# Optimization experiments

Measured on AMD Instinct MI355X. Metric: run time of the kernel, lower is better.

The kernel has to match this reference:

```python
import jax, jax.numpy as jnp
import numpy as np

E, T_MAX, H, L, V = 384, 256, 6, 6, 65
DH = E // H  # 64
EPS = 1e-5


def setup_inputs() -> dict:
    key = jax.random.key(0)
    ks = jax.random.split(key, 24)
    B, T = 128, 256
    s = 0.02
    inp = {
        "input_indices": jax.random.randint(ks[0], (B, T), 0, V, dtype=jnp.int64) if jax.config.read("jax_enable_x64") else jax.random.randint(ks[0], (B, T), 0, V, dtype=jnp.int32),
        "targets": jax.random.randint(ks[1], (B, T), 0, V, dtype=jnp.int32),
        "tok_emb": s * jax.random.normal(ks[2], (V, E), jnp.float32),
        "pos_emb": s * jax.random.normal(ks[3], (T_MAX, E), jnp.float32),
        "Wq": s * jax.random.normal(ks[4], (L, H, E, DH), jnp.float32),
        "Wk": s * jax.random.normal(ks[5], (L, H, E, DH), jnp.float32),
        "Wv": s * jax.random.normal(ks[6], (L, H, E, DH), jnp.float32),
        "Wo": s * jax.random.normal(ks[7], (L, E, E), jnp.float32),
        "bo": jnp.zeros((L, E), jnp.float32),
        "ln1_s": jnp.ones((L, E), jnp.float32),
        "ln1_b": jnp.zeros((L, E), jnp.float32),
        "ln2_s": jnp.ones((L, E), jnp.float32),
        "ln2_b": jnp.zeros((L, E), jnp.float32),
        "W1": s * jax.random.normal(ks[8], (L, E, 4 * E), jnp.float32),
        "b1": jnp.zeros((L, 4 * E), jnp.float32),
        "W2": s * jax.random.normal(ks[9], (L, 4 * E, E), jnp.float32),
        "b2": jnp.zeros((L, E), jnp.float32),
        "lnf_s": jnp.ones((E,), jnp.float32),
        "lnf_b": jnp.zeros((E,), jnp.float32),
        "Wout": s * jax.random.normal(ks[10], (E, V), jnp.float32),
        "bout": jnp.zeros((V,), jnp.float32),
    }
    return inp


def _ln(x, s, b):
    m = x.mean(-1, keepdims=True)
    v = ((x - m) ** 2).mean(-1, keepdims=True)
    return (x - m) * jax.lax.rsqrt(v + EPS) * s + b


def _forward(input_indices, targets, tok_emb, pos_emb, Wq, Wk, Wv, Wo, bo,
             ln1_s, ln1_b, ln2_s, ln2_b, W1, b1, W2, b2, lnf_s, lnf_b, Wout, bout):
    B, T = input_indices.shape
    x = tok_emb[input_indices] + pos_emb[:T]  # [B,T,E]
    causal = jnp.tril(jnp.ones((T, T), bool))
    scale = DH ** -0.5

    def block(x, p):
        wq, wk, wv, wo, bo_, l1s, l1b, l2s, l2b, w1, b1_, w2, b2_ = p
        h = _ln(x, l1s, l1b)
        q = jnp.einsum("bte,hed->bhtd", h, wq)
        k = jnp.einsum("bte,hed->bhtd", h, wk)
        v = jnp.einsum("bte,hed->bhtd", h, wv)
        scores = jnp.einsum("bhtd,bhsd->bhts", q, k) * scale
        scores = jnp.where(causal, scores, -jnp.inf)
        w = jax.nn.softmax(scores, axis=-1)
        att = jnp.einsum("bhts,bhsd->bhtd", w, v)  # [B,H,T,DH]
        att = att.transpose(0, 2, 1, 3).reshape(B, T, E)  # concat heads
        x = x + att @ wo + bo_
        h2 = _ln(x, l2s, l2b)
        ff = jax.nn.relu(h2 @ w1 + b1_) @ w2 + b2_
        return x + ff, None

    x, _ = jax.lax.scan(block, x, (Wq, Wk, Wv, Wo, bo, ln1_s, ln1_b, ln2_s, ln2_b, W1, b1, W2, b2))
    x = _ln(x, lnf_s, lnf_b)
    logits = x @ Wout + bout  # [B,T,V]
    logp = jax.nn.log_softmax(logits, axis=-1)
    nll = -jnp.take_along_axis(logp, targets[..., None], axis=-1)[..., 0]
    loss = nll.mean()
    return logits, loss


def reference(input_indices, targets, tok_emb, pos_emb, Wq, Wk, Wv, Wo, bo,
              ln1_s, ln1_b, ln2_s, ln2_b, W1, b1, W2, b2, lnf_s, lnf_b, Wout, bout):
    return _forward(input_indices, targets, tok_emb, pos_emb, Wq, Wk, Wv, Wo, bo,
                    ln1_s, ln1_b, ln2_s, ln2_b, W1, b1, W2, b2, lnf_s, lnf_b, Wout, bout)
```

## Files before the change

### kernel.cpp

```cpp
#include <hip/hip_runtime.h>

#define BT      32768
#define T_SEQ   256
#define E_DIM   384
#define NH      6
#define NL      6
#define VOC     65
#define FF_DIM  1536
#define QKV_N   1152

typedef short bf16x8 __attribute__((ext_vector_type(8)));
typedef float f32x4  __attribute__((ext_vector_type(4)));
typedef unsigned short u16;

typedef const unsigned int __attribute__((address_space(1))) gu32;
typedef unsigned int       __attribute__((address_space(3))) lu32;

__device__ __forceinline__ u16 f2bf(float x) {
  unsigned u = __builtin_bit_cast(unsigned, x);
  u += 0x7fffu + ((u >> 16) & 1u);
  return (u16)(u >> 16);
}
__device__ __forceinline__ float bf2f(u16 v) {
  unsigned u = ((unsigned)v) << 16;
  return __builtin_bit_cast(float, u);
}

__device__ __forceinline__ void load_lds_16(const void* g, void* l) {
  __builtin_amdgcn_global_load_lds((gu32*)g, (lu32*)l, 16, 0, 0);
}

__global__ __launch_bounds__(256) void transpose_t(
    const float* __restrict__ src, u16* __restrict__ dst, int R, int C,
    long sbs, long dbs_outer, int inner, long dbs_inner, long dbase) {
  __shared__ float t[32][33];
  const int b = blockIdx.z;
  const float* s = src + (long)b * sbs;
  u16* d = dst + dbase + (long)(b / inner) * dbs_outer + (long)(b % inner) * dbs_inner;
  const int r0 = blockIdx.x * 32, c0 = blockIdx.y * 32;
  const int tx = threadIdx.x & 31, ty = threadIdx.x >> 5;
#pragma unroll
  for (int i = 0; i < 4; i++) {
    int rr = ty + i * 8;
    int r = r0 + rr, c = c0 + tx;
    if (r < R && c < C) t[rr][tx] = s[(long)r * C + c];
  }
  __syncthreads();
#pragma unroll
  for (int i = 0; i < 4; i++) {
    int cc = ty + i * 8;
    int c = c0 + cc, r = r0 + tx;
    if (c < C && r < R) d[(long)c * R + r] = f2bf(t[tx][cc]);
  }
}

__global__ __launch_bounds__(256) void embed_k(const int* __restrict__ idx,
                                               const float* __restrict__ tok,
                                               const float* __restrict__ pos,
                                               u16* __restrict__ x) {
  int i = blockIdx.x * 256 + threadIdx.x;
  int bt = i / 48, q = i - bt * 48;
  int t = bt & 255;
  const float4* tp = (const float4*)(tok + (size_t)idx[bt] * E_DIM + q * 8);
  const float4* pp = (const float4*)(pos + (size_t)t * E_DIM + q * 8);
  float4 a0 = tp[0], a1 = tp[1], p0 = pp[0], p1 = pp[1];
  u16 o[8];
  o[0] = f2bf(a0.x + p0.x); o[1] = f2bf(a0.y + p0.y);
  o[2] = f2bf(a0.z + p0.z); o[3] = f2bf(a0.w + p0.w);
  o[4] = f2bf(a1.x + p1.x); o[5] = f2bf(a1.y + p1.y);
  o[6] = f2bf(a1.z + p1.z); o[7] = f2bf(a1.w + p1.w);
  *(bf16x8*)(x + (size_t)bt * E_DIM + q * 8) = *(bf16x8*)o;
}

__global__ __launch_bounds__(256) void ln_k(const u16* __restrict__ x,
                                            const float* __restrict__ gam,
                                            const float* __restrict__ bet,
                                            u16* __restrict__ out) {
  int tid = threadIdx.x, lane = tid & 63, w = tid >> 6;
  size_t token = (size_t)blockIdx.x * 4 + w;
  const u16* xr = x + token * E_DIM;
  u16 raw[6];
  *(uint2*)raw          = *(const uint2*)(xr + 4 * lane);
  *(unsigned*)(raw + 4) = *(const unsigned*)(xr + 256 + 2 * lane);
  float v[6]; float s = 0.f;
#pragma unroll
  for (int i = 0; i < 6; i++) { v[i] = bf2f(raw[i]); s += v[i]; }
#pragma unroll
  for (int d = 1; d < 64; d <<= 1) s += __shfl_xor(s, d);
  float mean = s * (1.f / E_DIM);
  float q = 0.f;
#pragma unroll
  for (int i = 0; i < 6; i++) { float d0 = v[i] - mean; q += d0 * d0; }
#pragma unroll
  for (int d = 1; d < 64; d <<= 1) q += __shfl_xor(q, d);
  float r = rsqrtf(q * (1.f / E_DIM) + 1e-5f);
  int e[6] = {4 * lane, 4 * lane + 1, 4 * lane + 2, 4 * lane + 3,
              256 + 2 * lane, 256 + 2 * lane + 1};
  u16 o[6];
#pragma unroll
  for (int i = 0; i < 6; i++)
    o[i] = f2bf((v[i] - mean) * r * gam[e[i]] + bet[e[i]]);
  u16* orow = out + token * E_DIM;
  *(uint2*)(orow + 4 * lane)          = *(uint2*)o;
  *(unsigned*)(orow + 256 + 2 * lane) = *(unsigned*)(o + 4);
}

__global__ __launch_bounds__(256) void gemm_d(
    const u16* __restrict__ A, const u16* __restrict__ Bt, int K, int Nstore,
    const float* __restrict__ bias, const u16* __restrict__ resid,
    u16* __restrict__ outH, float* __restrict__ outF, int relu) {
  __shared__ u16 smem[16384];
  u16* As = smem;
  u16* Bs = smem + 8192;
  const int tid = threadIdx.x, lane = tid & 63, wv = tid >> 6;
  const int quad = lane >> 4, l16 = lane & 15;
  const int m0 = blockIdx.x * 128, n0 = blockIdx.y * 128;
  const int wm = (wv & 1) * 64, wn = (wv >> 1) * 64;

  const int lrow = lane >> 2;
  const int lchunk = (lane & 3) ^ ((lane >> 3) & 3);

  f32x4 acc[4][4];
#pragma unroll
  for (int i = 0; i < 4; i++)
#pragma unroll
    for (int j = 0; j < 4; j++) acc[i][j] = (f32x4){0.f, 0.f, 0.f, 0.f};

  auto stage = [&](int sel, int k0) {
#pragma unroll
    for (int j = 0; j < 2; j++) {
      int rid = wv * 2 + j;
      int r = rid * 16 + lrow;
      load_lds_16(A + (size_t)(m0 + r) * K + k0 + lchunk * 8, &As[sel * 4096 + rid * 512]);
      load_lds_16(Bt + (size_t)(n0 + r) * K + k0 + lchunk * 8, &Bs[sel * 4096 + rid * 512]);
    }
  };

  const int NK = K >> 5;
  stage(0, 0);
  __syncthreads();
  const int slot = (quad ^ ((l16 >> 1) & 3)) * 8;
  for (int kt = 0; kt < NK; kt++) {
    const int cur = kt & 1;
    if (kt + 1 < NK) stage(cur ^ 1, (kt + 1) * 32);
    const u16* Ab = As + cur * 4096;
    const u16* Bb = Bs + cur * 4096;
    bf16x8 af[4], bfr[4];
#pragma unroll
    for (int i = 0; i < 4; i++) af[i]  = *(const bf16x8*)&Ab[(wm + i * 16 + l16) * 32 + slot];
#pragma unroll
    for (int j = 0; j < 4; j++) bfr[j] = *(const bf16x8*)&Bb[(wn + j * 16 + l16) * 32 + slot];
#pragma unroll
    for (int i = 0; i < 4; i++)
#pragma unroll
      for (int j = 0; j < 4; j++)
        acc[i][j] = __builtin_amdgcn_mfma_f32_16x16x32_bf16(af[i], bfr[j], acc[i][j], 0, 0, 0);
    __syncthreads();
  }

  if (outH) {
#pragma unroll
    for (int p = 0; p < 4; p++) {
      if (p) __syncthreads();
      if ((wv >> 1) == (p >> 1)) {
#pragma unroll
        for (int jj = 0; jj < 2; jj++) {
          int j = (p & 1) * 2 + jj;
          int gn = n0 + wn + j * 16 + l16;
          float bv = bias ? bias[gn] : 0.f;
          int lcol = jj * 16 + l16;
#pragma unroll
          for (int i = 0; i < 4; i++)
#pragma unroll
            for (int r = 0; r < 4; r++) {
              float v = acc[i][j][r] + bv;
              if (relu) v = fmaxf(v, 0.f);
              smem[(wm + i * 16 + quad * 4 + r) * 36 + lcol] = f2bf(v);
            }
        }
      }
      __syncthreads();
      const int gc0 = n0 + p * 32;
#pragma unroll
      for (int s = 0; s < 4; s++) {
        int row = s * 32 + (tid >> 3);
        int seg = (tid & 7) * 4;
        u16 pk[4];
        *(uint2*)pk = *(const uint2*)&smem[row * 36 + seg];
        size_t o = (size_t)(m0 + row) * Nstore + gc0 + seg;
        if (resid) {
          u16 rv[4];
          *(uint2*)rv = *(const uint2*)&resid[o];
#pragma unroll
          for (int q2 = 0; q2 < 4; q2++) pk[q2] = f2bf(bf2f(pk[q2]) + bf2f(rv[q2]));
        }
        *(uint2*)&outH[o] = *(uint2*)pk;
      }
    }
  } else {
#pragma unroll
    for (int j = 0; j < 4; j++) {
      const int gn = n0 + wn + j * 16 + l16;
      if (gn < Nstore) {
        const float bv = bias ? bias[gn] : 0.f;
#pragma unroll
        for (int i = 0; i < 4; i++)
#pragma unroll
          for (int r = 0; r < 4; r++) {
            const int gm = m0 + wm + i * 16 + quad * 4 + r;
            outF[(size_t)gm * Nstore + gn] = acc[i][j][r] + bv;
          }
      }
    }
  }
}

__global__ __launch_bounds__(512) void attn_k(const u16* __restrict__ qkv,
                                              u16* __restrict__ att) {
  __shared__ u16 Kc[64 * 64];
  __shared__ u16 Vtc[64 * 64];
  __shared__ u16 Pl[8 * 16 * 64];
  const int b = blockIdx.x / NH, h = blockIdx.x % NH;
  const int tid = threadIdx.x, lane = tid & 63, w = tid >> 6;
  const int quad = lane >> 4, l16 = lane & 15;
  const int rowb = b * T_SEQ;
  const int tiles[2] = {w, 15 - w};

  bf16x8 qf[2][2];
#pragma unroll
  for (int ti = 0; ti < 2; ti++)
#pragma unroll
    for (int kk = 0; kk < 2; kk++)
      qf[ti][kk] = *(const bf16x8*)(qkv + (size_t)(rowb + tiles[ti] * 16 + l16) * QKV_N +
                                    h * 64 + kk * 32 + quad * 8);

  f32x4 Oa[2][4];
  float mrun[2][4], lrun[2][4];
#pragma unroll
  for (int ti = 0; ti < 2; ti++) {
#pragma unroll
    for (int di = 0; di < 4; di++) Oa[ti][di] = (f32x4){0.f, 0.f, 0.f, 0.f};
#pragma unroll
    for (int r = 0; r < 4; r++) { mrun[ti][r] = -1e30f; lrun[ti][r] = 0.f; }
  }

  u16* Pw = &Pl[w * 1024];
  const int sr = tid >> 3, sseg = tid & 7;
  const int kst = sseg ^ (sr & 7) ^ ((sr >> 3) & 7);

  for (int c = 0; c < 4; c++) {
    const int s0 = c * 64;
    __syncthreads();
    *(uint4*)&Kc[sr * 64 + kst * 8] =
        *(const uint4*)(qkv + (size_t)(rowb + s0 + sr) * QKV_N + 384 + h * 64 + sseg * 8);
    {
      union { uint4 u; u16 us[8]; } tb;
      tb.u = *(const uint4*)(qkv + (size_t)(rowb + s0 + sr) * QKV_N + 768 + h * 64 + sseg * 8);
#pragma unroll
      for (int j = 0; j < 8; j++) {
        int d = sseg * 8 + j;
        int vst = (sr >> 3) ^ (d & 7) ^ ((d >> 3) & 7);
        Vtc[d * 64 + vst * 8 + (sr & 7)] = tb.us[j];
      }
    }
    __syncthreads();

    bf16x8 kf[4][2], vf[4][2];
    bool loaded = false;
#pragma unroll
    for (int ti = 0; ti < 2; ti++) {
      const int t = tiles[ti];
      if (t < 4 * c) continue;
      if (!loaded) {
        loaded = true;
#pragma unroll
        for (int ni = 0; ni < 4; ni++)
#pragma unroll
          for (int kk = 0; kk < 2; kk++) {
            int srow = ni * 16 + l16;
            int ks = (kk * 4 + quad) ^ (srow & 7) ^ ((srow >> 3) & 7);
            kf[ni][kk] = *(const bf16x8*)&Kc[srow * 64 + ks * 8];
            int drow = ni * 16 + l16;
            int vs = (kk * 4 + quad) ^ (drow & 7) ^ ((drow >> 3) & 7);
            vf[ni][kk] = *(const bf16x8*)&Vtc[drow * 64 + vs * 8];
          }
      }
      f32x4 S[4];
#pragma unroll
      for (int ni = 0; ni < 4; ni++) {
        f32x4 z = (f32x4){0.f, 0.f, 0.f, 0.f};
        z = __builtin_amdgcn_mfma_f32_16x16x32_bf16(qf[ti][0], kf[ni][0], z, 0, 0, 0);
        S[ni] = __builtin_amdgcn_mfma_f32_16x16x32_bf16(qf[ti][1], kf[ni][1], z, 0, 0, 0);
      }
      const bool diag = ((t >> 2) == c);
#pragma unroll
      for (int ni = 0; ni < 4; ni++)
#pragma unroll
        for (int r = 0; r < 4; r++) {
          float xv = S[ni][r] * 0.125f;
          if (diag) {
            int trow = t * 16 + quad * 4 + r;
            int s = s0 + ni * 16 + l16;
            if (s > trow) xv = -1e30f;
          }
          S[ni][r] = xv;
        }
#pragma unroll
      for (int r = 0; r < 4; r++) {
        float mx = fmaxf(fmaxf(S[0][r], S[1][r]), fmaxf(S[2][r], S[3][r]));
        mx = fmaxf(mx, __shfl_xor(mx, 1));
        mx = fmaxf(mx, __shfl_xor(mx, 2));
        mx = fmaxf(mx, __shfl_xor(mx, 4));
        mx = fmaxf(mx, __shfl_xor(mx, 8));
        float mnew = fmaxf(mrun[ti][r], mx);
        float alpha = __expf(mrun[ti][r] - mnew);
        float ls = 0.f;
#pragma unroll
        for (int ni = 0; ni < 4; ni++) {
          float p = __expf(S[ni][r] - mnew);
          S[ni][r] = p; ls += p;
        }
        ls += __shfl_xor(ls, 1); ls += __shfl_xor(ls, 2);
        ls += __shfl_xor(ls, 4); ls += __shfl_xor(ls, 8);
        lrun[ti][r] = lrun[ti][r] * alpha + ls;
        mrun[ti][r] = mnew;
#pragma unroll
        for (int di = 0; di < 4; di++) Oa[ti][di][r] *= alpha;
      }
#pragma unroll
      for (int ni = 0; ni < 4; ni++)
#pragma unroll
        for (int r = 0; r < 4; r++) {
          int ch = 2 * ni + (l16 >> 3);
          int st = ch ^ (quad | ((r & 1) << 2));
          Pw[(quad * 4 + r) * 64 + st * 8 + (l16 & 7)] = f2bf(S[ni][r]);
        }
      bf16x8 pf[2];
#pragma unroll
      for (int kk = 0; kk < 2; kk++) {
        int key = (l16 >> 2) | ((l16 & 1) << 2);
        int st = (kk * 4 + quad) ^ key;
        pf[kk] = *(const bf16x8*)&Pw[l16 * 64 + st * 8];
      }
#pragma unroll
      for (int di = 0; di < 4; di++) {
        Oa[ti][di] = __builtin_amdgcn_mfma_f32_16x16x32_bf16(pf[0], vf[di][0], Oa[ti][di], 0, 0, 0);
        Oa[ti][di] = __builtin_amdgcn_mfma_f32_16x16x32_bf16(pf[1], vf[di][1], Oa[ti][di], 0, 0, 0);
      }
    }
  }

#pragma unroll
  for (int ti = 0; ti < 2; ti++)
#pragma unroll
    for (int r = 0; r < 4; r++) {
      float inv = 1.f / lrun[ti][r];
      int trow = tiles[ti] * 16 + quad * 4 + r;
#pragma unroll
      for (int di = 0; di < 4; di++)
        att[(size_t)(rowb + trow) * E_DIM + h * 64 + di * 16 + l16] = f2bf(Oa[ti][di][r] * inv);
    }
}

__global__ __launch_bounds__(256) void loss_k(const float* __restrict__ logits,
                                              const int* __restrict__ tgt,
                                              float* __restrict__ loss) {
  __shared__ float part[4];
  const int tid = threadIdx.x, lane = tid & 63, w = tid >> 6;
  const int wave_id = blockIdx.x * 4 + w;
  float acc = 0.f;
  for (int t = wave_id; t < BT; t += 2048) {
    const float* row = logits + (size_t)t * VOC;
    float a = row[lane];
    float b = (lane == 0) ? row[64] : -1e30f;
    float mx = fmaxf(a, b);
#pragma unroll
    for (int d = 1; d < 64; d <<= 1) mx = fmaxf(mx, __shfl_xor(mx, d));
    float sum = __expf(a - mx) + ((lane == 0) ? __expf(b - mx) : 0.f);
#pragma unroll
    for (int d = 1; d < 64; d <<= 1) sum += __shfl_xor(sum, d);
    if (lane == 0) acc += mx + __logf(sum) - row[tgt[t]];
  }
  if (lane == 0) part[w] = acc;
  __syncthreads();
  if (tid == 0)
    atomicAdd(loss, (part[0] + part[1] + part[2] + part[3]) * (1.f / (float)BT));
}

extern "C" void kernel_launch(void* const* d_in, const int* in_sizes, int n_in,
                              void* d_out, int out_size, void* d_ws, size_t ws_size,
                              hipStream_t stream) {
  (void)in_sizes; (void)n_in; (void)out_size; (void)ws_size;
  const int*   idx  = (const int*)d_in[0];
  const int*   tgt  = (const int*)d_in[1];
  const float* tok  = (const float*)d_in[2];
  const float* pos  = (const float*)d_in[3];
  const float* Wq   = (const float*)d_in[4];
  const float* Wk   = (const float*)d_in[5];
  const float* Wv   = (const float*)d_in[6];
  const float* Wo   = (const float*)d_in[7];
  const float* bo   = (const float*)d_in[8];
  const float* ln1s = (const float*)d_in[9];
  const float* ln1b = (const float*)d_in[10];
  const float* ln2s = (const float*)d_in[11];
  const float* ln2b = (const float*)d_in[12];
  const float* W1   = (const float*)d_in[13];
  const float* b1   = (const float*)d_in[14];
  const float* W2   = (const float*)d_in[15];
  const float* b2   = (const float*)d_in[16];
  const float* lnfs = (const float*)d_in[17];
  const float* lnfb = (const float*)d_in[18];
  const float* Wout = (const float*)d_in[19];
  const float* bout = (const float*)d_in[20];

  char* w = (char*)d_ws;
  u16* x      = (u16*)w;    w += (size_t)BT * E_DIM * 2;
  u16* hb     = (u16*)w;    w += (size_t)BT * E_DIM * 2;
  u16* attb   = (u16*)w;    w += (size_t)BT * E_DIM * 2;
  u16* big    = (u16*)w;    w += (size_t)BT * FF_DIM * 2;
  u16* Wqkv_t = (u16*)w;    w += (size_t)NL * QKV_N * E_DIM * 2;
  u16* Wo_t   = (u16*)w;    w += (size_t)NL * E_DIM * E_DIM * 2;
  u16* W1_t   = (u16*)w;    w += (size_t)NL * FF_DIM * E_DIM * 2;
  u16* W2_t   = (u16*)w;    w += (size_t)NL * E_DIM * FF_DIM * 2;
  u16* Wout_t = (u16*)w;    w += (size_t)128 * E_DIM * 2;
  u16* qkv = big;
  u16* ff  = big;

  float* logits = (float*)d_out;
  float* loss   = logits + (size_t)BT * VOC;

  hipMemsetAsync(Wout_t, 0, 128 * E_DIM * 2, stream);
  transpose_t<<<dim3(12, 2, 36), 256, 0, stream>>>(Wq, Wqkv_t, 384, 64,
      24576, 442368, 6, 24576, 0);
  transpose_t<<<dim3(12, 2, 36), 256, 0, stream>>>(Wk, Wqkv_t, 384, 64,
      24576, 442368, 6, 24576, (long)384 * 384);
  transpose_t<<<dim3(12, 2, 36), 256, 0, stream>>>(Wv, Wqkv_t, 384, 64,
      24576, 442368, 6, 24576, (long)768 * 384);
  transpose_t<<<dim3(12, 12, 6), 256, 0, stream>>>(Wo, Wo_t, 384, 384,
      147456, 147456, 1, 0, 0);
  transpose_t<<<dim3(12, 48, 6), 256, 0, stream>>>(W1, W1_t, 384, 1536,
      589824, 589824, 1, 0, 0);
  transpose_t<<<dim3(48, 12, 6), 256, 0, stream>>>(W2, W2_t, 1536, 384,
      589824, 589824, 1, 0, 0);
  transpose_t<<<dim3(12, 3, 1), 256, 0, stream>>>(Wout, Wout_t, 384, 65,
      0, 0, 1, 0, 0);

  embed_k<<<6144, 256, 0, stream>>>(idx, tok, pos, x);

  for (int l = 0; l < NL; l++) {
    ln_k<<<8192, 256, 0, stream>>>(x, ln1s + l * E_DIM, ln1b + l * E_DIM, hb);
    gemm_d<<<dim3(256, 9), 256, 0, stream>>>(hb, Wqkv_t + (size_t)l * QKV_N * E_DIM,
                                             384, QKV_N, nullptr, nullptr, qkv, nullptr, 0);
    attn_k<<<768, 512, 0, stream>>>(qkv, attb);
    gemm_d<<<dim3(256, 3), 256, 0, stream>>>(attb, Wo_t + (size_t)l * E_DIM * E_DIM,
                                             384, E_DIM, bo + l * E_DIM, x, x, nullptr, 0);
    ln_k<<<8192, 256, 0, stream>>>(x, ln2s + l * E_DIM, ln2b + l * E_DIM, hb);
    gemm_d<<<dim3(256, 12), 256, 0, stream>>>(hb, W1_t + (size_t)l * FF_DIM * E_DIM,
                                              384, FF_DIM, b1 + l * FF_DIM, nullptr, ff, nullptr, 1);
    gemm_d<<<dim3(256, 3), 256, 0, stream>>>(ff, W2_t + (size_t)l * E_DIM * FF_DIM,
                                             1536, E_DIM, b2 + l * E_DIM, x, x, nullptr, 0);
  }
  ln_k<<<8192, 256, 0, stream>>>(x, lnfs, lnfb, hb);
  gemm_d<<<dim3(256, 1), 256, 0, stream>>>(hb, Wout_t, 384, VOC, bout, nullptr, nullptr, logits, 0);

  hipMemsetAsync(loss, 0, 4, stream);
  loss_k<<<512, 256, 0, stream>>>(logits, tgt, loss);
}
```

Before: 1.800 ms.

## Give each wave private LDS tiles to remove block barriers in GEMM loop

The GEMM kernel now has each wave stage its own A and B sub-tiles into a private LDS region, so the per-iteration __syncthreads is replaced by per-wave s_waitcnt vmcnt waits with a prefetch two K-steps ahead. This removes block-wide barriers from the main loop. In exchange, LDS use doubles to 64KB per block, which lowers occupancy, and A/B rows shared between waves are now loaded redundantly (twice each). The attention change is a cosmetic variable reuse.

After: 2.247 ms. 1.25x slower.

```diff
diff --git a/kernel.cpp b/kernel.cpp
--- a/kernel.cpp
+++ b/kernel.cpp
@@ -105,17 +105,16 @@
   *(unsigned*)(orow + 256 + 2 * lane) = *(unsigned*)(o + 4);
 }
 
-__global__ __launch_bounds__(256) void gemm_d(
+__global__ __launch_bounds__(256) void gemm_w(
     const u16* __restrict__ A, const u16* __restrict__ Bt, int K, int Nstore,
     const float* __restrict__ bias, const u16* __restrict__ resid,
     u16* __restrict__ outH, float* __restrict__ outF, int relu) {
-  __shared__ u16 smem[16384];
-  u16* As = smem;
-  u16* Bs = smem + 8192;
+  __shared__ u16 smem[32768];
   const int tid = threadIdx.x, lane = tid & 63, wv = tid >> 6;
   const int quad = lane >> 4, l16 = lane & 15;
   const int m0 = blockIdx.x * 128, n0 = blockIdx.y * 128;
   const int wm = (wv & 1) * 64, wn = (wv >> 1) * 64;
+  u16* WB = smem + wv * 8192;
 
   const int lrow = lane >> 2;
   const int lchunk = (lane & 3) ^ ((lane >> 3) & 3);
@@ -128,40 +127,40 @@
 
   auto stage = [&](int sel, int k0) {
 #pragma unroll
-    for (int j = 0; j < 2; j++) {
-      int rid = wv * 2 + j;
-      int r = rid * 16 + lrow;
-      load_lds_16(A + (size_t)(m0 + r) * K + k0 + lchunk * 8, &As[sel * 4096 + rid * 512]);
-      load_lds_16(Bt + (size_t)(n0 + r) * K + k0 + lchunk * 8, &Bs[sel * 4096 + rid * 512]);
+    for (int j = 0; j < 4; j++) {
+      load_lds_16(A  + (size_t)(m0 + wm + j * 16 + lrow) * K + k0 + lchunk * 8,
+                  WB + sel * 2048 + j * 512);
+      load_lds_16(Bt + (size_t)(n0 + wn + j * 16 + lrow) * K + k0 + lchunk * 8,
+                  WB + 4096 + sel * 2048 + j * 512);
     }
   };
 
   const int NK = K >> 5;
   stage(0, 0);
-  __syncthreads();
+  if (NK > 1) stage(1, 32);
   const int slot = (quad ^ ((l16 >> 1) & 3)) * 8;
   for (int kt = 0; kt < NK; kt++) {
-    const int cur = kt & 1;
-    if (kt + 1 < NK) stage(cur ^ 1, (kt + 1) * 32);
-    const u16* Ab = As + cur * 4096;
-    const u16* Bb = Bs + cur * 4096;
+    if (kt + 1 < NK) asm volatile("s_waitcnt vmcnt(8)" ::: "memory");
+    else             asm volatile("s_waitcnt vmcnt(0)" ::: "memory");
+    const u16* Ab = WB + (kt & 1) * 2048;
+    const u16* Bb = WB + 4096 + (kt & 1) * 2048;
     bf16x8 af[4], bfr[4];
 #pragma unroll
-    for (int i = 0; i < 4; i++) af[i]  = *(const bf16x8*)&Ab[(wm + i * 16 + l16) * 32 + slot];
-#pragma unroll
-    for (int j = 0; j < 4; j++) bfr[j] = *(const bf16x8*)&Bb[(wn + j * 16 + l16) * 32 + slot];
+    for (int i = 0; i < 4; i++) af[i]  = *(const bf16x8*)&Ab[(i * 16 + l16) * 32 + slot];
+#pragma unroll
+    for (int j = 0; j < 4; j++) bfr[j] = *(const bf16x8*)&Bb[(j * 16 + l16) * 32 + slot];
 #pragma unroll
     for (int i = 0; i < 4; i++)
 #pragma unroll
       for (int j = 0; j < 4; j++)
         acc[i][j] = __builtin_amdgcn_mfma_f32_16x16x32_bf16(af[i], bfr[j], acc[i][j], 0, 0, 0);
-    __syncthreads();
+    if (kt + 2 < NK) stage(kt & 1, (kt + 2) * 32);
   }
 
   if (outH) {
 #pragma unroll
     for (int p = 0; p < 4; p++) {
-      if (p) __syncthreads();
+      __syncthreads();
       if ((wv >> 1) == (p >> 1)) {
 #pragma unroll
         for (int jj = 0; jj < 2; jj++) {
@@ -280,9 +279,8 @@
             int srow = ni * 16 + l16;
             int ks = (kk * 4 + quad) ^ (srow & 7) ^ ((srow >> 3) & 7);
             kf[ni][kk] = *(const bf16x8*)&Kc[srow * 64 + ks * 8];
-            int drow = ni * 16 + l16;
-            int vs = (kk * 4 + quad) ^ (drow & 7) ^ ((drow >> 3) & 7);
-            vf[ni][kk] = *(const bf16x8*)&Vtc[drow * 64 + vs * 8];
+            int vs = (kk * 4 + quad) ^ (srow & 7) ^ ((srow >> 3) & 7);
+            vf[ni][kk] = *(const bf16x8*)&Vtc[srow * 64 + vs * 8];
           }
       }
       f32x4 S[4];
@@ -449,19 +447,19 @@
 
   for (int l = 0; l < NL; l++) {
     ln_k<<<8192, 256, 0, stream>>>(x, ln1s + l * E_DIM, ln1b + l * E_DIM, hb);
-    gemm_d<<<dim3(256, 9), 256, 0, stream>>>(hb, Wqkv_t + (size_t)l * QKV_N * E_DIM,
+    gemm_w<<<dim3(256, 9), 256, 0, stream>>>(hb, Wqkv_t + (size_t)l * QKV_N * E_DIM,
                                              384, QKV_N, nullptr, nullptr, qkv, nullptr, 0);
     attn_k<<<768, 512, 0, stream>>>(qkv, attb);
-    gemm_d<<<dim3(256, 3), 256, 0, stream>>>(attb, Wo_t + (size_t)l * E_DIM * E_DIM,
+    gemm_w<<<dim3(256, 3), 256, 0, stream>>>(attb, Wo_t + (size_t)l * E_DIM * E_DIM,
                                              384, E_DIM, bo + l * E_DIM, x, x, nullptr, 0);
     ln_k<<<8192, 256, 0, stream>>>(x, ln2s + l * E_DIM, ln2b + l * E_DIM, hb);
-    gemm_d<<<dim3(256, 12), 256, 0, stream>>>(hb, W1_t + (size_t)l * FF_DIM * E_DIM,
+    gemm_w<<<dim3(256, 12), 256, 0, stream>>>(hb, W1_t + (size_t)l * FF_DIM * E_DIM,
                                               384, FF_DIM, b1 + l * FF_DIM, nullptr, ff, nullptr, 1);
-    gemm_d<<<dim3(256, 3), 256, 0, stream>>>(ff, W2_t + (size_t)l * E_DIM * FF_DIM,
+    gemm_w<<<dim3(256, 3), 256, 0, stream>>>(ff, W2_t + (size_t)l * E_DIM * FF_DIM,
                                              1536, E_DIM, b2 + l * E_DIM, x, x, nullptr, 0);
   }
   ln_k<<<8192, 256, 0, stream>>>(x, lnfs, lnfb, hb);
-  gemm_d<<<dim3(256, 1), 256, 0, stream>>>(hb, Wout_t, 384, VOC, bout, nullptr, nullptr, logits, 0);
+  gemm_w<<<dim3(256, 1), 256, 0, stream>>>(hb, Wout_t, 384, VOC, bout, nullptr, nullptr, logits, 0);
 
   hipMemsetAsync(loss, 0, 4, stream);
   loss_k<<<512, 256, 0, stream>>>(logits, tgt, loss);
```
